# Kernel tuning notes

Hardware: AMD Instinct MI355X
Metric: run time of the kernel (lower is better)

The kernel has to match this reference:

```python
import jax, jax.numpy as jnp
import numpy as np


def conv1d(x, w, b, pad):
    # x: (B, Cin, T), w: (Cout, Cin, K), b: (Cout,)
    y = jax.lax.conv_general_dilated(x, w, window_strides=(1,), padding=[(pad, pad)],
                                     dimension_numbers=('NCH', 'OIH', 'NCH'))
    return y + b[None, :, None]


def setup_inputs() -> dict:
    key = jax.random.key(0)
    ks = jax.random.split(key, 16)
    B, Cmel, Ctxt, Catt, T1, T2 = 16, 80, 256, 80, 800, 200
    s = 0.05
    return {
        'queries': jax.random.normal(ks[0], (B, Cmel, T1), jnp.float32),
        'keys': jax.random.normal(ks[1], (B, Ctxt, T2), jnp.float32),
        'attn_prior': jax.random.uniform(ks[2], (B, T1, T2), jnp.float32),
        # key_proj: Conv1d(256->512,k=3,pad=1) -> ReLU -> Conv1d(512->80,k=1)
        'kw1': jax.random.normal(ks[3], (Ctxt * 2, Ctxt, 3), jnp.float32) * s,
        'kb1': jax.random.normal(ks[4], (Ctxt * 2,), jnp.float32) * s,
        'kw2': jax.random.normal(ks[5], (Catt, Ctxt * 2, 1), jnp.float32) * s,
        'kb2': jax.random.normal(ks[6], (Catt,), jnp.float32) * s,
        # query_proj (3xconv): 80->160 k3 -> ReLU -> 160->80 k1 -> ReLU -> 80->80 k1
        'qw1': jax.random.normal(ks[7], (Cmel * 2, Cmel, 3), jnp.float32) * s,
        'qb1': jax.random.normal(ks[8], (Cmel * 2,), jnp.float32) * s,
        'qw2': jax.random.normal(ks[9], (Cmel, Cmel * 2, 1), jnp.float32) * s,
        'qb2': jax.random.normal(ks[10], (Cmel,), jnp.float32) * s,
        'qw3': jax.random.normal(ks[11], (Catt, Cmel, 1), jnp.float32) * s,
        'qb3': jax.random.normal(ks[12], (Catt,), jnp.float32) * s,
    }


def reference(queries, keys, attn_prior, kw1, kb1, kw2, kb2, qw1, qb1, qw2, qb2, qw3, qb3):
    # key encoder
    k = jax.nn.relu(conv1d(keys, kw1, kb1, pad=1))
    k = conv1d(k, kw2, kb2, pad=0)                      # (B, Catt, T2)
    # query encoder ('3xconv')
    q = jax.nn.relu(conv1d(queries, qw1, qb1, pad=1))
    q = jax.nn.relu(conv1d(q, qw2, qb2, pad=0))
    q = conv1d(q, qw3, qb3, pad=0)                      # (B, Catt, T1)
    # L2 distance over channels: ||q||^2 + ||k||^2 - 2 q.k (same math as broadcast (q-k)^2 sum)
    q2 = jnp.sum(q * q, axis=1)                         # (B, T1)
    k2 = jnp.sum(k * k, axis=1)                         # (B, T2)
    qk = jnp.einsum('bct,bcs->bts', q, k)               # (B, T1, T2)
    attn = -0.0005 * (q2[:, :, None] + k2[:, None, :] - 2.0 * qk)[:, None]  # (B,1,T1,T2)
    attn = jax.nn.log_softmax(attn, axis=3) + jnp.log(attn_prior[:, None] + 1e-8)
    return attn
```

## Files before the change

kernel.cpp:

```cpp
#include <hip/hip_runtime.h>
#include <cstdint>
#include <cmath>

using short8  = __attribute__((ext_vector_type(8))) short;
using short4v = __attribute__((ext_vector_type(4))) short;
using floatx4 = __attribute__((ext_vector_type(4))) float;

__device__ __forceinline__ short f2bf(float f) {
  union { float f; unsigned u; } x; x.f = f;
  unsigned r = x.u + 0x7FFFu + ((x.u >> 16) & 1u);
  return (short)(r >> 16);
}

__device__ __forceinline__ void gl_lds16(const short* g, short* l) {
  __builtin_amdgcn_global_load_lds(
      (const __attribute__((address_space(1))) void*)g,
      (__attribute__((address_space(3))) void*)l, 16, 0, 0);
}

__global__ __launch_bounds__(256) void prep_kernel(
    const float* __restrict__ keys, const float* __restrict__ queries,
    const float* __restrict__ kw1, const float* __restrict__ kw2,
    const float* __restrict__ qw1, const float* __restrict__ qw2,
    const float* __restrict__ qw3,
    short* __restrict__ kT0, short* __restrict__ qT0,
    short* __restrict__ w1, short* __restrict__ w2, short* __restrict__ w3,
    short* __restrict__ w4, short* __restrict__ w5)
{
  const int bid = blockIdx.x, tid = threadIdx.x;
  __shared__ float xs[32][65];

  if (bid < 1136) {
    const float* src; short* dst; int CIN, T, CP, bx, by, b;
    if (bid < 512) {
      src = keys; dst = kT0; CIN = 256; T = 200; CP = 256;
      bx = bid & 3; by = (bid >> 2) & 7; b = bid >> 5;
    } else {
      int b2 = bid - 512;
      src = queries; dst = qT0; CIN = 80; T = 800; CP = 96;
      bx = b2 % 13; by = (b2 / 13) % 3; b = b2 / 39;
    }
    const int t0 = bx * 64, ci0 = by * 32;
    for (int i = tid; i < 32 * 64; i += 256) {
      int row = i >> 6, col = i & 63;
      float v = 0.f;
      if (ci0 + row < CIN && t0 + col < T)
        v = src[((size_t)b * CIN + ci0 + row) * T + t0 + col];
      xs[row][col] = v;
    }
    __syncthreads();
    int t = tid >> 2, c8 = (tid & 3) * 8;
    if (t0 + t < T) {
      short8 o;
      #pragma unroll
      for (int j = 0; j < 8; ++j) o[j] = f2bf(xs[c8 + j][t]);
      *(short8*)&dst[((size_t)b * T + t0 + t) * CP + ci0 + c8] = o;
    }
  } else {
    int blk = bid - 1136;
    const float* src; short* dst; int base;
    int CoP, CiP, Cout, CIN, K; bool isW1 = false;
    if      (blk < 384) { src=kw1; dst=w1; base=0;   CoP=512; CiP=256; Cout=512; CIN=256; K=3; isW1=true; }
    else if (blk < 432) { src=kw2; dst=w2; base=384; CoP=96;  CiP=512; Cout=80;  CIN=512; K=1; }
    else if (blk < 486) { src=qw1; dst=w3; base=432; CoP=192; CiP=96;  Cout=160; CIN=80;  K=3; }
    else if (blk < 504) { src=qw2; dst=w4; base=486; CoP=96;  CiP=192; Cout=80;  CIN=160; K=1; }
    else                { src=qw3; dst=w5; base=504; CoP=96;  CiP=96;  Cout=80;  CIN=80;  K=1; }
    int tot = K * CoP * CiP;
    int b0 = (blk - base) * 1024;
    for (int e = 0; e < 4; ++e) {
      int gi = b0 + e * 256 + tid;
      if (gi < tot) {
        int dk  = gi / (CoP * CiP);
        int rem = gi - dk * (CoP * CiP);
        int co  = rem / CiP, ci = rem - (rem / CiP) * CiP;
        float v = (co < Cout && ci < CIN) ? src[((size_t)co * CIN + ci) * K + dk] : 0.f;
        int idx = gi;
        if (isW1) idx = (((ci >> 5) * 3 + dk) * 512 + co) * 32 + (ci & 31);
        dst[idx] = f2bf(v);
      }
    }
  }
}

__global__ __launch_bounds__(256) void conv_k3_kernel(
    const short* __restrict__ kT0, const short* __restrict__ qT0,
    const short* __restrict__ w1, const short* __restrict__ w3,
    const short* __restrict__ w4, const short* __restrict__ w5,
    const float* __restrict__ kb1, const float* __restrict__ qb1,
    const float* __restrict__ qb2, const float* __restrict__ qb3,
    short* __restrict__ kT1, short* __restrict__ qF)
{
  __shared__ __align__(16) short smem[23040];
  const int tid = threadIdx.x, wid = tid >> 6, lane = tid & 63;
  const int q = lane >> 4, m = lane & 15;

  if (blockIdx.x < 512) {
    const int blk = blockIdx.x;
    const int bb = blk >> 5, co0 = ((blk >> 2) & 7) * 64, t0 = (blk & 3) * 64;
    const int wy = wid >> 1, wx = wid & 1;
    const int wv = tid >> 6;

    floatx4 acc[2][2];
    #pragma unroll
    for (int i = 0; i < 2; ++i)
      #pragma unroll
      for (int j = 0; j < 2; ++j) acc[i][j] = (floatx4){0.f, 0.f, 0.f, 0.f};

    auto xload = [&](int c0s, int4& a, int4& bvv) {
      { int row = tid >> 2, g = tid & 3;
        int t = t0 + row - 1;
        a = (int4){0,0,0,0};
        if (t >= 0 && t < 200)
          a = *(const int4*)&kT0[((size_t)bb * 200 + t) * 256 + c0s * 32 + g * 8]; }
      bvv = (int4){0,0,0,0};
      if (tid < 8) {
        int i1 = tid + 256, row = i1 >> 2, g = i1 & 3;
        int t = t0 + row - 1;
        if (t >= 0 && t < 200)
          bvv = *(const int4*)&kT0[((size_t)bb * 200 + t) * 256 + c0s * 32 + g * 8];
      }
    };
    auto xstore = [&](const int4& a, const int4& bvv, int xoff) {
      { int row = tid >> 2, g = tid & 3; *(int4*)&smem[xoff + row * 40 + g * 8] = a; }
      if (tid < 8) { int i1 = tid + 256, row = i1 >> 2, g = i1 & 3;
        *(int4*)&smem[xoff + row * 40 + g * 8] = bvv; }
    };
    auto wissue = [&](int c0s, int aoff) {
      #pragma unroll
      for (int c = 0; c < 3; ++c) {
        const short* g = w1 + ((size_t)(c0s * 3 + c) * 512 + co0) * 32 + tid * 8;
        gl_lds16(g, &smem[aoff + c * 2048 + wv * 512]);
      }
    };

    { int4 a, bvv; xload(0, a, bvv); wissue(0, 5280); xstore(a, bvv, 0); }
    __syncthreads();

    int cur = 0;
    for (int c0 = 0; c0 < 8; ++c0) {
      const int xo = cur ? 2640 : 0;
      const int ao = cur ? 11424 : 5280;
      int4 xa, xb;
      if (c0 < 7) {
        wissue(c0 + 1, cur ? 5280 : 11424);
        xload(c0 + 1, xa, xb);
      }
      #pragma unroll
      for (int dk = 0; dk < 3; ++dk) {
        short8 fa0 = *(const short8*)&smem[ao + dk * 2048 + (wy * 32 + m) * 32 + q * 8];
        short8 fa1 = *(const short8*)&smem[ao + dk * 2048 + (wy * 32 + 16 + m) * 32 + q * 8];
        #pragma unroll
        for (int j = 0; j < 2; ++j) {
          short8 fb = *(const short8*)&smem[xo + (wx * 32 + j * 16 + m + dk) * 40 + q * 8];
          acc[0][j] = __builtin_amdgcn_mfma_f32_16x16x32_bf16(fa0, fb, acc[0][j], 0, 0, 0);
          acc[1][j] = __builtin_amdgcn_mfma_f32_16x16x32_bf16(fa1, fb, acc[1][j], 0, 0, 0);
        }
      }
      if (c0 < 7) {
        xstore(xa, xb, cur ? 0 : 2640);
        __syncthreads();
      }
      cur ^= 1;
    }
    #pragma unroll
    for (int i = 0; i < 2; ++i) {
      #pragma unroll
      for (int j = 0; j < 2; ++j) {
        #pragma unroll
        for (int r = 0; r < 4; ++r) {
          int co = co0 + wy * 32 + i * 16 + q * 4 + r;
          int t  = t0 + wx * 32 + j * 16 + m;
          if (t < 200) {
            float v = fmaxf(acc[i][j][r] + kb1[co], 0.f);
            kT1[((size_t)bb * 200 + t) * 512 + co] = f2bf(v);
          }
        }
      }
    }
  } else {
    const int qbid = blockIdx.x - 512;
    const int b = qbid / 13, t0 = (qbid % 13) * 64;
    short* xs2 = smem;
    short* y1c = smem + 7680;
    short* y2c = smem;

    floatx4 accq[3][4];
    #pragma unroll
    for (int f = 0; f < 3; ++f)
      #pragma unroll
      for (int tf = 0; tf < 4; ++tf) accq[f][tf] = (floatx4){0.f, 0.f, 0.f, 0.f};

    for (int i = tid; i < 66 * 12; i += 256) {
      int row = i / 12, g = i - (i / 12) * 12;
      int t = t0 + row - 1;
      int4 v = {0, 0, 0, 0};
      if (t >= 0 && t < 800)
        v = *(const int4*)&qT0[((size_t)b * 800 + t) * 96 + g * 8];
      *(int4*)&xs2[row * 104 + g * 8] = v;
    }
    __syncthreads();

    for (int c0 = 0; c0 < 3; ++c0) {
      #pragma unroll
      for (int dk = 0; dk < 3; ++dk) {
        short8 fa[3];
        #pragma unroll
        for (int f = 0; f < 3; ++f)
          fa[f] = *(const short8*)&w3[((size_t)(dk * 192 + wid * 48 + f * 16 + m)) * 96
                                      + c0 * 32 + q * 8];
        #pragma unroll
        for (int tf = 0; tf < 4; ++tf) {
          short8 fb = *(const short8*)&xs2[(tf * 16 + m + dk) * 104 + c0 * 32 + q * 8];
          #pragma unroll
          for (int f = 0; f < 3; ++f)
            accq[f][tf] = __builtin_amdgcn_mfma_f32_16x16x32_bf16(fa[f], fb, accq[f][tf], 0, 0, 0);
        }
      }
    }
    __syncthreads();
    #pragma unroll
    for (int f = 0; f < 3; ++f) {
      #pragma unroll
      for (int tf = 0; tf < 4; ++tf) {
        int co = wid * 48 + f * 16 + q * 4;
        int t  = tf * 16 + m;
        short4v o;
        #pragma unroll
        for (int r = 0; r < 4; ++r) {
          float bv = (co + r < 160) ? qb1[co + r] : 0.f;
          o[r] = f2bf(fmaxf(accq[f][tf][r] + bv, 0.f));
        }
        *(short4v*)&y1c[(co >> 5) * 2560 + t * 40 + (co & 31)] = o;
      }
    }
    __syncthreads();

    floatx4 acc2q[6];
    #pragma unroll
    for (int f = 0; f < 6; ++f) acc2q[f] = (floatx4){0.f, 0.f, 0.f, 0.f};
    #pragma unroll
    for (int c = 0; c < 6; ++c) {
      short8 fb = *(const short8*)&y1c[c * 2560 + (wid * 16 + m) * 40 + q * 8];
      #pragma unroll
      for (int f = 0; f < 6; ++f) {
        short8 fa = *(const short8*)&w4[((size_t)(f * 16 + m)) * 192 + c * 32 + q * 8];
        acc2q[f] = __builtin_amdgcn_mfma_f32_16x16x32_bf16(fa, fb, acc2q[f], 0, 0, 0);
      }
    }
    #pragma unroll
    for (int f = 0; f < 6; ++f) {
      int co = f * 16 + q * 4;
      int t  = wid * 16 + m;
      short4v o;
      #pragma unroll
      for (int r = 0; r < 4; ++r) {
        float bv = (co + r < 80) ? qb2[co + r] : 0.f;
        o[r] = f2bf(fmaxf(acc2q[f][r] + bv, 0.f));
      }
      *(short4v*)&y2c[(co >> 5) * 2560 + t * 40 + (co & 31)] = o;
    }
    __syncthreads();

    floatx4 acc3q[6];
    #pragma unroll
    for (int f = 0; f < 6; ++f) acc3q[f] = (floatx4){0.f, 0.f, 0.f, 0.f};
    #pragma unroll
    for (int c = 0; c < 3; ++c) {
      short8 fb = *(const short8*)&y2c[c * 2560 + (wid * 16 + m) * 40 + q * 8];
      #pragma unroll
      for (int f = 0; f < 6; ++f) {
        short8 fa = *(const short8*)&w5[((size_t)(f * 16 + m)) * 96 + c * 32 + q * 8];
        acc3q[f] = __builtin_amdgcn_mfma_f32_16x16x32_bf16(fa, fb, acc3q[f], 0, 0, 0);
      }
    }
    int t = t0 + wid * 16 + m;
    if (t < 800) {
      #pragma unroll
      for (int f = 0; f < 6; ++f) {
        int co = f * 16 + q * 4;
        short4v o;
        #pragma unroll
        for (int r = 0; r < 4; ++r) {
          float bv = (co + r < 80) ? qb3[co + r] : 0.f;
          o[r] = f2bf(acc3q[f][r] + bv);
        }
        *(short4v*)&qF[((size_t)b * 800 + t) * 96 + co] = o;
      }
    }
  }
}

__global__ __launch_bounds__(64) void kconv2_kernel(
    const short* __restrict__ kT1, const short* __restrict__ w2,
    const float* __restrict__ kb2, short* __restrict__ kF)
{
  const int blk = blockIdx.x;
  const int b = blk / 13, t0 = (blk - b * 13) * 16;
  const int lane = threadIdx.x & 63;
  const int q = lane >> 4, m = lane & 15;
  const int t = t0 + m;
  const bool tv = (t < 200);

  floatx4 acc[6];
  #pragma unroll
  for (int f = 0; f < 6; ++f) acc[f] = (floatx4){0.f, 0.f, 0.f, 0.f};

  #pragma unroll
  for (int c = 0; c < 16; ++c) {
    short8 fb;
    if (tv) fb = *(const short8*)&kT1[((size_t)b * 200 + t) * 512 + c * 32 + q * 8];
    else    fb = (short8){0,0,0,0,0,0,0,0};
    #pragma unroll
    for (int f = 0; f < 6; ++f) {
      short8 fa = *(const short8*)&w2[((size_t)(f * 16 + m)) * 512 + c * 32 + q * 8];
      acc[f] = __builtin_amdgcn_mfma_f32_16x16x32_bf16(fa, fb, acc[f], 0, 0, 0);
    }
  }
  if (tv) {
    #pragma unroll
    for (int f = 0; f < 6; ++f) {
      int co = f * 16 + q * 4;
      short4v o;
      #pragma unroll
      for (int r = 0; r < 4; ++r) {
        float bv = (co + r < 80) ? kb2[co + r] : 0.f;
        o[r] = f2bf(acc[f][r] + bv);
      }
      *(short4v*)&kF[((size_t)b * 200 + t) * 96 + co] = o;
    }
  }
}

__global__ __launch_bounds__(256) void attn_mfma(
    const short* __restrict__ qT, const short* __restrict__ kT,
    const float* __restrict__ prior, float* __restrict__ out)
{
  const int b = blockIdx.y, t1_0 = blockIdx.x * 64;
  const int tid = threadIdx.x, wid = tid >> 6, lane = tid & 63;
  const int q = lane >> 4, m = lane & 15;

  __shared__ __align__(16) char smem[51200];
  short* aq = (short*)smem;
  short* bk = (short*)(smem + 13312);
  float* k2s = (float*)(smem + 29952);
  float* sstage = (float*)smem;

  floatx4 acc[13];
  #pragma unroll
  for (int f = 0; f < 13; ++f) acc[f] = (floatx4){0.f, 0.f, 0.f, 0.f};

  for (int i = tid; i < 64 * 12; i += 256) {
    int row = i / 12, g = i - (i / 12) * 12;
    int4 v = {0, 0, 0, 0};
    if (t1_0 + row < 800)
      v = *(const int4*)&qT[((size_t)b * 800 + t1_0 + row) * 96 + g * 8];
    *(int4*)&aq[row * 104 + g * 8] = v;
  }

  float k2acc = 0.f;
  for (int c = 0; c < 3; ++c) {
    __syncthreads();
    for (int i = tid; i < 208 * 4; i += 256) {
      int row = i >> 2, g = i & 3;
      int4 v = {0, 0, 0, 0};
      if (row < 200)
        v = *(const int4*)&kT[((size_t)b * 200 + row) * 96 + c * 32 + g * 8];
      *(int4*)&bk[row * 40 + g * 8] = v;
    }
    __syncthreads();
    if (tid < 208) {
      #pragma unroll
      for (int g = 0; g < 4; ++g) {
        short8 s = *(const short8*)&bk[tid * 40 + g * 8];
        #pragma unroll
        for (int j = 0; j < 8; ++j) {
          union { unsigned u; float f; } x; x.u = ((unsigned)(unsigned short)s[j]) << 16;
          k2acc = fmaf(x.f, x.f, k2acc);
        }
      }
    }
    short8 fa = *(const short8*)&aq[(wid * 16 + m) * 104 + c * 32 + q * 8];
    #pragma unroll
    for (int f = 0; f < 13; ++f) {
      short8 fb = *(const short8*)&bk[(f * 16 + m) * 40 + q * 8];
      acc[f] = __builtin_amdgcn_mfma_f32_16x16x32_bf16(fa, fb, acc[f], 0, 0, 0);
    }
  }
  if (tid < 208) k2s[tid] = k2acc;
  __syncthreads();

  float k2v[13];
  #pragma unroll
  for (int f = 0; f < 13; ++f) k2v[f] = k2s[f * 16 + m];

  float mx[4] = {-INFINITY, -INFINITY, -INFINITY, -INFINITY};
  #pragma unroll
  for (int f = 0; f < 13; ++f) {
    bool valid = (f * 16 + m) < 200;
    #pragma unroll
    for (int r = 0; r < 4; ++r) {
      float v = valid ? (0.001f * acc[f][r] - 0.0005f * k2v[f]) : -INFINITY;
      acc[f][r] = v;
      mx[r] = fmaxf(mx[r], v);
    }
  }
  #pragma unroll
  for (int msk = 1; msk < 16; msk <<= 1)
    #pragma unroll
    for (int r = 0; r < 4; ++r) mx[r] = fmaxf(mx[r], __shfl_xor(mx[r], msk));
  float sm[4] = {0.f, 0.f, 0.f, 0.f};
  #pragma unroll
  for (int f = 0; f < 13; ++f)
    #pragma unroll
    for (int r = 0; r < 4; ++r) sm[r] += __expf(acc[f][r] - mx[r]);
  #pragma unroll
  for (int msk = 1; msk < 16; msk <<= 1)
    #pragma unroll
    for (int r = 0; r < 4; ++r) sm[r] += __shfl_xor(sm[r], msk);
  float lse[4];
  #pragma unroll
  for (int r = 0; r < 4; ++r) lse[r] = mx[r] + __logf(sm[r]);

  __syncthreads();
  #pragma unroll
  for (int f = 0; f < 13; ++f) {
    int col = f * 16 + m;
    if (col < 200) {
      #pragma unroll
      for (int r = 0; r < 4; ++r)
        sstage[(wid * 16 + q * 4 + r) * 200 + col] = acc[f][r] - lse[r];
    }
  }
  __syncthreads();

  for (int i = tid; i < 64 * 50; i += 256) {
    int row = i / 50, seg = i - (i / 50) * 50;
    int t1 = t1_0 + row;
    if (t1 < 800) {
      size_t o = ((size_t)b * 800 + t1) * 200 + seg * 4;
      floatx4 pv = *(const floatx4*)&prior[o];
      floatx4 sv = *(const floatx4*)&sstage[row * 200 + seg * 4];
      floatx4 ov;
      #pragma unroll
      for (int j = 0; j < 4; ++j) ov[j] = sv[j] + __logf(pv[j] + 1e-8f);
      *(floatx4*)&out[o] = ov;
    }
  }
}

extern "C" void kernel_launch(void* const* d_in, const int* in_sizes, int n_in,
                              void* d_out, int out_size, void* d_ws, size_t ws_size,
                              hipStream_t stream) {
  const float* queries = (const float*)d_in[0];
  const float* keys    = (const float*)d_in[1];
  const float* prior   = (const float*)d_in[2];
  const float* kw1 = (const float*)d_in[3];
  const float* kb1 = (const float*)d_in[4];
  const float* kw2 = (const float*)d_in[5];
  const float* kb2 = (const float*)d_in[6];
  const float* qw1 = (const float*)d_in[7];
  const float* qb1 = (const float*)d_in[8];
  const float* qw2 = (const float*)d_in[9];
  const float* qb2 = (const float*)d_in[10];
  const float* qw3 = (const float*)d_in[11];
  const float* qb3 = (const float*)d_in[12];
  float* out = (float*)d_out;

  short* p = (short*)d_ws;
  short* kT0 = p;  p += (size_t)3200 * 256;
  short* qT0 = p;  p += (size_t)12800 * 96;
  short* w1  = p;  p += (size_t)3 * 512 * 256;
  short* w2  = p;  p += (size_t)96 * 512;
  short* w3  = p;  p += (size_t)3 * 192 * 96;
  short* w4  = p;  p += (size_t)96 * 192;
  short* w5  = p;  p += (size_t)96 * 96;
  short* kT1 = p;  p += (size_t)3200 * 512;
  short* kF  = p;  p += (size_t)3200 * 96;
  short* qF  = p;  p += (size_t)12800 * 96;

  prep_kernel<<<dim3(1649), 256, 0, stream>>>(keys, queries, kw1, kw2, qw1, qw2, qw3,
                                              kT0, qT0, w1, w2, w3, w4, w5);
  conv_k3_kernel<<<dim3(720), 256, 0, stream>>>(kT0, qT0, w1, w3, w4, w5,
                                                kb1, qb1, qb2, qb3, kT1, qF);
  kconv2_kernel<<<dim3(208), 64, 0, stream>>>(kT1, w2, kb2, kF);
  attn_mfma<<<dim3(13, 16), 256, 0, stream>>>(qF, kF, prior, out);
}
```

Baseline: 140.0 us.

## Compute key norms in kconv2 epilogue and halve attention tile rows

The squared key norms are now computed once in the kconv2 epilogue from the bf16-rounded outputs and written to a global buffer. Previously every attention block recomputed them from LDS. The attention kernel now handles 32 query rows per block with 128 threads, giving 400 blocks instead of 208 and halving shared memory per block. Since 800 divides evenly by 32, bounds checks on query rows are dropped. The cost is an extra global buffer and a load of the norms per lane, while more blocks should fill the GPU's compute units better.

Result: no change. 141.3 us (+0.9%).

```diff
diff --git a/kernel.cpp b/kernel.cpp
--- a/kernel.cpp
+++ b/kernel.cpp
@@ -10,6 +10,11 @@
   union { float f; unsigned u; } x; x.f = f;
   unsigned r = x.u + 0x7FFFu + ((x.u >> 16) & 1u);
   return (short)(r >> 16);
+}
+
+__device__ __forceinline__ float bf2f(short s) {
+  union { unsigned u; float f; } x; x.u = ((unsigned)(unsigned short)s) << 16;
+  return x.f;
 }
 
 __device__ __forceinline__ void gl_lds16(const short* g, short* l) {
@@ -292,7 +297,8 @@
 
 __global__ __launch_bounds__(64) void kconv2_kernel(
     const short* __restrict__ kT1, const short* __restrict__ w2,
-    const float* __restrict__ kb2, short* __restrict__ kF)
+    const float* __restrict__ kb2, short* __restrict__ kF,
+    float* __restrict__ k2g)
 {
   const int blk = blockIdx.x;
   const int b = blk / 13, t0 = (blk - b * 13) * 16;
@@ -317,6 +323,7 @@
     }
   }
   if (tv) {
+    float k2acc = 0.f;
     #pragma unroll
     for (int f = 0; f < 6; ++f) {
       int co = f * 16 + q * 4;
@@ -324,43 +331,46 @@
       #pragma unroll
       for (int r = 0; r < 4; ++r) {
         float bv = (co + r < 80) ? kb2[co + r] : 0.f;
-        o[r] = f2bf(acc[f][r] + bv);
+        short s = f2bf(acc[f][r] + bv);
+        o[r] = s;
+        float vb = bf2f(s);
+        k2acc = fmaf(vb, vb, k2acc);
       }
       *(short4v*)&kF[((size_t)b * 200 + t) * 96 + co] = o;
     }
-  }
-}
-
-__global__ __launch_bounds__(256) void attn_mfma(
+    k2acc += __shfl_xor(k2acc, 16);
+    k2acc += __shfl_xor(k2acc, 32);
+    if (q == 0) k2g[b * 200 + t] = k2acc;
+  }
+}
+
+__global__ __launch_bounds__(128) void attn_mfma(
     const short* __restrict__ qT, const short* __restrict__ kT,
-    const float* __restrict__ prior, float* __restrict__ out)
+    const float* __restrict__ k2g, const float* __restrict__ prior,
+    float* __restrict__ out)
 {
-  const int b = blockIdx.y, t1_0 = blockIdx.x * 64;
+  const int b = blockIdx.y, t1_0 = blockIdx.x * 32;
   const int tid = threadIdx.x, wid = tid >> 6, lane = tid & 63;
   const int q = lane >> 4, m = lane & 15;
 
-  __shared__ __align__(16) char smem[51200];
+  __shared__ __align__(16) char smem[25600];
   short* aq = (short*)smem;
-  short* bk = (short*)(smem + 13312);
-  float* k2s = (float*)(smem + 29952);
+  short* bk = (short*)(smem + 6656);
   float* sstage = (float*)smem;
 
   floatx4 acc[13];
   #pragma unroll
   for (int f = 0; f < 13; ++f) acc[f] = (floatx4){0.f, 0.f, 0.f, 0.f};
 
-  for (int i = tid; i < 64 * 12; i += 256) {
+  for (int i = tid; i < 32 * 12; i += 128) {
     int row = i / 12, g = i - (i / 12) * 12;
-    int4 v = {0, 0, 0, 0};
-    if (t1_0 + row < 800)
-      v = *(const int4*)&qT[((size_t)b * 800 + t1_0 + row) * 96 + g * 8];
-    *(int4*)&aq[row * 104 + g * 8] = v;
-  }
-
-  float k2acc = 0.f;
+    *(int4*)&aq[row * 104 + g * 8] =
+        *(const int4*)&qT[((size_t)b * 800 + t1_0 + row) * 96 + g * 8];
+  }
+
   for (int c = 0; c < 3; ++c) {
     __syncthreads();
-    for (int i = tid; i < 208 * 4; i += 256) {
+    for (int i = tid; i < 208 * 4; i += 128) {
       int row = i >> 2, g = i & 3;
       int4 v = {0, 0, 0, 0};
       if (row < 200)
@@ -368,17 +378,6 @@
       *(int4*)&bk[row * 40 + g * 8] = v;
     }
     __syncthreads();
-    if (tid < 208) {
-      #pragma unroll
-      for (int g = 0; g < 4; ++g) {
-        short8 s = *(const short8*)&bk[tid * 40 + g * 8];
-        #pragma unroll
-        for (int j = 0; j < 8; ++j) {
-          union { unsigned u; float f; } x; x.u = ((unsigned)(unsigned short)s[j]) << 16;
-          k2acc = fmaf(x.f, x.f, k2acc);
-        }
-      }
-    }
     short8 fa = *(const short8*)&aq[(wid * 16 + m) * 104 + c * 32 + q * 8];
     #pragma unroll
     for (int f = 0; f < 13; ++f) {
@@ -386,12 +385,13 @@
       acc[f] = __builtin_amdgcn_mfma_f32_16x16x32_bf16(fa, fb, acc[f], 0, 0, 0);
     }
   }
-  if (tid < 208) k2s[tid] = k2acc;
-  __syncthreads();
 
   float k2v[13];
   #pragma unroll
-  for (int f = 0; f < 13; ++f) k2v[f] = k2s[f * 16 + m];
+  for (int f = 0; f < 13; ++f) {
+    int col = f * 16 + m;
+    k2v[f] = (col < 200) ? k2g[b * 200 + col] : 0.f;
+  }
 
   float mx[4] = {-INFINITY, -INFINITY, -INFINITY, -INFINITY};
   #pragma unroll
@@ -433,18 +433,15 @@
   }
   __syncthreads();
 
-  for (int i = tid; i < 64 * 50; i += 256) {
+  for (int i = tid; i < 32 * 50; i += 128) {
     int row = i / 50, seg = i - (i / 50) * 50;
-    int t1 = t1_0 + row;
-    if (t1 < 800) {
-      size_t o = ((size_t)b * 800 + t1) * 200 + seg * 4;
-      floatx4 pv = *(const floatx4*)&prior[o];
-      floatx4 sv = *(const floatx4*)&sstage[row * 200 + seg * 4];
-      floatx4 ov;
-      #pragma unroll
-      for (int j = 0; j < 4; ++j) ov[j] = sv[j] + __logf(pv[j] + 1e-8f);
-      *(floatx4*)&out[o] = ov;
-    }
+    size_t o = ((size_t)b * 800 + t1_0 + row) * 200 + seg * 4;
+    floatx4 pv = *(const floatx4*)&prior[o];
+    floatx4 sv = *(const floatx4*)&sstage[row * 200 + seg * 4];
+    floatx4 ov;
+    #pragma unroll
+    for (int j = 0; j < 4; ++j) ov[j] = sv[j] + __logf(pv[j] + 1e-8f);
+    *(floatx4*)&out[o] = ov;
   }
 }
 
@@ -477,11 +474,12 @@
   short* kT1 = p;  p += (size_t)3200 * 512;
   short* kF  = p;  p += (size_t)3200 * 96;
   short* qF  = p;  p += (size_t)12800 * 96;
+  float* k2g = (float*)p;
 
   prep_kernel<<<dim3(1649), 256, 0, stream>>>(keys, queries, kw1, kw2, qw1, qw2, qw3,
                                               kT0, qT0, w1, w2, w3, w4, w5);
   conv_k3_kernel<<<dim3(720), 256, 0, stream>>>(kT0, qT0, w1, w3, w4, w5,
                                                 kb1, qb1, qb2, qb3, kT1, qF);
-  kconv2_kernel<<<dim3(208), 64, 0, stream>>>(kT1, w2, kb2, kF);
-  attn_mfma<<<dim3(13, 16), 256, 0, stream>>>(qF, kF, prior, out);
-}
+  kconv2_kernel<<<dim3(208), 64, 0, stream>>>(kT1, w2, kb2, kF, k2g);
+  attn_mfma<<<dim3(25, 16), 128, 0, stream>>>(qF, kF, k2g, prior, out);
+}
```

## Fuse key 1x1 conv into attention kernel, computing key features in LDS

Applied to the files above, without the earlier changes.

Removes the separate kconv2 kernel launch and its kF round trip through global memory. Each attention block now computes the full 200x80 key projection for its batch straight into shared memory, then runs the QK MFMA and k2 norms from LDS. The cost is redundant work: the key 1x1 conv is recomputed by all 13 blocks that share a batch, and LDS use grows, which may lower occupancy.

Measured after the change: 171.5 us. 1.22x slower.

```diff
diff --git a/kernel.cpp b/kernel.cpp
--- a/kernel.cpp
+++ b/kernel.cpp
@@ -10,6 +10,11 @@
   union { float f; unsigned u; } x; x.f = f;
   unsigned r = x.u + 0x7FFFu + ((x.u >> 16) & 1u);
   return (short)(r >> 16);
+}
+
+__device__ __forceinline__ float bf2f(short s) {
+  union { unsigned u; float f; } x; x.u = ((unsigned)(unsigned short)s) << 16;
+  return x.f;
 }
 
 __device__ __forceinline__ void gl_lds16(const short* g, short* l) {
@@ -290,65 +295,25 @@
   }
 }
 
-__global__ __launch_bounds__(64) void kconv2_kernel(
-    const short* __restrict__ kT1, const short* __restrict__ w2,
-    const float* __restrict__ kb2, short* __restrict__ kF)
-{
-  const int blk = blockIdx.x;
-  const int b = blk / 13, t0 = (blk - b * 13) * 16;
-  const int lane = threadIdx.x & 63;
-  const int q = lane >> 4, m = lane & 15;
-  const int t = t0 + m;
-  const bool tv = (t < 200);
-
-  floatx4 acc[6];
-  #pragma unroll
-  for (int f = 0; f < 6; ++f) acc[f] = (floatx4){0.f, 0.f, 0.f, 0.f};
-
-  #pragma unroll
-  for (int c = 0; c < 16; ++c) {
-    short8 fb;
-    if (tv) fb = *(const short8*)&kT1[((size_t)b * 200 + t) * 512 + c * 32 + q * 8];
-    else    fb = (short8){0,0,0,0,0,0,0,0};
-    #pragma unroll
-    for (int f = 0; f < 6; ++f) {
-      short8 fa = *(const short8*)&w2[((size_t)(f * 16 + m)) * 512 + c * 32 + q * 8];
-      acc[f] = __builtin_amdgcn_mfma_f32_16x16x32_bf16(fa, fb, acc[f], 0, 0, 0);
-    }
-  }
-  if (tv) {
-    #pragma unroll
-    for (int f = 0; f < 6; ++f) {
-      int co = f * 16 + q * 4;
-      short4v o;
-      #pragma unroll
-      for (int r = 0; r < 4; ++r) {
-        float bv = (co + r < 80) ? kb2[co + r] : 0.f;
-        o[r] = f2bf(acc[f][r] + bv);
-      }
-      *(short4v*)&kF[((size_t)b * 200 + t) * 96 + co] = o;
-    }
-  }
-}
-
-__global__ __launch_bounds__(256) void attn_mfma(
-    const short* __restrict__ qT, const short* __restrict__ kT,
+__global__ __launch_bounds__(256) void attn_fused(
+    const short* __restrict__ qT, const short* __restrict__ kT1,
+    const short* __restrict__ w2, const float* __restrict__ kb2,
     const float* __restrict__ prior, float* __restrict__ out)
 {
   const int b = blockIdx.y, t1_0 = blockIdx.x * 64;
   const int tid = threadIdx.x, wid = tid >> 6, lane = tid & 63;
   const int q = lane >> 4, m = lane & 15;
 
-  __shared__ __align__(16) char smem[51200];
-  short* aq = (short*)smem;
-  short* bk = (short*)(smem + 13312);
-  float* k2s = (float*)(smem + 29952);
+  __shared__ __align__(16) char smem[57408];
+  short* kFl = (short*)smem;
+  short* aq  = (short*)(smem + 43264);
+  float* k2s = (float*)(smem + 56576);
   float* sstage = (float*)smem;
 
-  floatx4 acc[13];
-  #pragma unroll
-  for (int f = 0; f < 13; ++f) acc[f] = (floatx4){0.f, 0.f, 0.f, 0.f};
-
+  for (int i = tid; i < 8 * 13; i += 256) {
+    int row = 200 + i / 13, g = i - (i / 13) * 13;
+    *(int4*)&kFl[row * 104 + g * 8] = (int4){0, 0, 0, 0};
+  }
   for (int i = tid; i < 64 * 12; i += 256) {
     int row = i / 12, g = i - (i / 12) * 12;
     int4 v = {0, 0, 0, 0};
@@ -357,36 +322,67 @@
     *(int4*)&aq[row * 104 + g * 8] = v;
   }
 
-  float k2acc = 0.f;
+  for (int gi = 0; gi < 4; ++gi) {
+    int g = wid + gi * 4;
+    if (g > 12) break;
+    int t2 = g * 16 + m;
+    bool tv = (t2 < 200);
+
+    floatx4 acc6[6];
+    #pragma unroll
+    for (int f = 0; f < 6; ++f) acc6[f] = (floatx4){0.f, 0.f, 0.f, 0.f};
+    #pragma unroll
+    for (int c = 0; c < 16; ++c) {
+      short8 fb;
+      if (tv) fb = *(const short8*)&kT1[((size_t)b * 200 + t2) * 512 + c * 32 + q * 8];
+      else    fb = (short8){0,0,0,0,0,0,0,0};
+      #pragma unroll
+      for (int f = 0; f < 6; ++f) {
+        short8 fa = *(const short8*)&w2[((size_t)(f * 16 + m)) * 512 + c * 32 + q * 8];
+        acc6[f] = __builtin_amdgcn_mfma_f32_16x16x32_bf16(fa, fb, acc6[f], 0, 0, 0);
+      }
+    }
+    if (tv) {
+      #pragma unroll
+      for (int f = 0; f < 6; ++f) {
+        int co = f * 16 + q * 4;
+        short4v o;
+        #pragma unroll
+        for (int r = 0; r < 4; ++r) {
+          float bv = (co + r < 80) ? kb2[co + r] : 0.f;
+          o[r] = f2bf(acc6[f][r] + bv);
+        }
+        *(short4v*)&kFl[t2 * 104 + co] = o;
+      }
+    }
+  }
+  __syncthreads();
+
+  floatx4 acc[13];
+  #pragma unroll
+  for (int f = 0; f < 13; ++f) acc[f] = (floatx4){0.f, 0.f, 0.f, 0.f};
+  #pragma unroll
   for (int c = 0; c < 3; ++c) {
-    __syncthreads();
-    for (int i = tid; i < 208 * 4; i += 256) {
-      int row = i >> 2, g = i & 3;
-      int4 v = {0, 0, 0, 0};
-      if (row < 200)
-        v = *(const int4*)&kT[((size_t)b * 200 + row) * 96 + c * 32 + g * 8];
-      *(int4*)&bk[row * 40 + g * 8] = v;
-    }
-    __syncthreads();
-    if (tid < 208) {
-      #pragma unroll
-      for (int g = 0; g < 4; ++g) {
-        short8 s = *(const short8*)&bk[tid * 40 + g * 8];
-        #pragma unroll
-        for (int j = 0; j < 8; ++j) {
-          union { unsigned u; float f; } x; x.u = ((unsigned)(unsigned short)s[j]) << 16;
-          k2acc = fmaf(x.f, x.f, k2acc);
-        }
-      }
-    }
     short8 fa = *(const short8*)&aq[(wid * 16 + m) * 104 + c * 32 + q * 8];
     #pragma unroll
     for (int f = 0; f < 13; ++f) {
-      short8 fb = *(const short8*)&bk[(f * 16 + m) * 40 + q * 8];
+      short8 fb = *(const short8*)&kFl[(f * 16 + m) * 104 + c * 32 + q * 8];
       acc[f] = __builtin_amdgcn_mfma_f32_16x16x32_bf16(fa, fb, acc[f], 0, 0, 0);
     }
   }
-  if (tid < 208) k2s[tid] = k2acc;
+  if (tid < 208) {
+    float k2acc = 0.f;
+    #pragma unroll
+    for (int g = 0; g < 12; ++g) {
+      short8 s = *(const short8*)&kFl[tid * 104 + g * 8];
+      #pragma unroll
+      for (int j = 0; j < 8; ++j) {
+        float v = bf2f(s[j]);
+        k2acc = fmaf(v, v, k2acc);
+      }
+    }
+    k2s[tid] = k2acc;
+  }
   __syncthreads();
 
   float k2v[13];
@@ -475,13 +471,11 @@
   short* w4  = p;  p += (size_t)96 * 192;
   short* w5  = p;  p += (size_t)96 * 96;
   short* kT1 = p;  p += (size_t)3200 * 512;
-  short* kF  = p;  p += (size_t)3200 * 96;
   short* qF  = p;  p += (size_t)12800 * 96;
 
   prep_kernel<<<dim3(1649), 256, 0, stream>>>(keys, queries, kw1, kw2, qw1, qw2, qw3,
                                               kT0, qT0, w1, w2, w3, w4, w5);
   conv_k3_kernel<<<dim3(720), 256, 0, stream>>>(kT0, qT0, w1, w3, w4, w5,
                                                 kb1, qb1, qb2, qb3, kT1, qF);
-  kconv2_kernel<<<dim3(208), 64, 0, stream>>>(kT1, w2, kb2, kF);
-  attn_mfma<<<dim3(13, 16), 256, 0, stream>>>(qF, kF, prior, out);
-}
+  attn_fused<<<dim3(13, 16), 256, 0, stream>>>(qF, kT1, w2, kb2, prior, out);
+}
```
